# Kernel optimization log

Hardware: AMD Instinct MI355X
Metric: run time of the kernel (lower is better)

Reference implementation:

```python
import jax, jax.numpy as jnp
import numpy as np

N = 50000      # nodes
E = 800000     # edges (before self loops)
D_IN = 128
HID = 64
HEADS = 8
D_OUT = 10


def setup_inputs() -> dict:
    key = jax.random.key(0)
    ks = jax.random.split(key, 16)
    sc = 0.05
    x = jax.random.normal(ks[0], (N, D_IN), dtype=jnp.float32)
    edge_index = jax.random.randint(ks[1], (2, E), 0, N, dtype=jnp.int64)
    return {
        "x": x,
        "edge_index": edge_index,
        "W1": jax.random.normal(ks[2], (HEADS * HID, D_IN), dtype=jnp.float32) * sc,
        "a1_src": jax.random.normal(ks[3], (HEADS, HID), dtype=jnp.float32) * sc,
        "a1_dst": jax.random.normal(ks[4], (HEADS, HID), dtype=jnp.float32) * sc,
        "b1": jnp.zeros((HEADS * HID,), jnp.float32),
        "W2": jax.random.normal(ks[5], (HID, HEADS * HID), dtype=jnp.float32) * sc,
        "a2_src": jax.random.normal(ks[6], (1, HID), dtype=jnp.float32) * sc,
        "a2_dst": jax.random.normal(ks[7], (1, HID), dtype=jnp.float32) * sc,
        "b2": jnp.zeros((HID,), jnp.float32),
        "W3": jax.random.normal(ks[8], (HID, HID), dtype=jnp.float32) * sc,
        "a3_src": jax.random.normal(ks[9], (1, HID), dtype=jnp.float32) * sc,
        "a3_dst": jax.random.normal(ks[10], (1, HID), dtype=jnp.float32) * sc,
        "b3": jnp.zeros((HID,), jnp.float32),
        "Wc": jax.random.normal(ks[11], (D_OUT, HID), dtype=jnp.float32) * sc,
        "bc": jnp.zeros((D_OUT,), jnp.float32),
    }


def gat_conv(x, src, dst, W, a_src, a_dst, b, concat):
    """PyG GATConv (eval mode, add_self_loops already applied to src/dst)."""
    heads, out_ch = a_src.shape
    n = x.shape[0]
    h = (x @ W.T).reshape(n, heads, out_ch)          # [N, H, C]
    a_s = jnp.einsum('nhc,hc->nh', h, a_src)          # [N, H]
    a_d = jnp.einsum('nhc,hc->nh', h, a_dst)          # [N, H]
    e = jax.nn.leaky_relu(a_s[src] + a_d[dst], 0.2)   # [Etot, H]
    # segment softmax over incoming edges of each destination node
    m = jax.ops.segment_max(e, dst, num_segments=n)
    ex = jnp.exp(e - m[dst])
    s = jax.ops.segment_sum(ex, dst, num_segments=n)
    alpha = ex / (s[dst] + 1e-16)                     # [Etot, H]
    out = jax.ops.segment_sum(h[src] * alpha[:, :, None], dst, num_segments=n)
    if concat:
        out = out.reshape(n, heads * out_ch)
    else:
        out = out.mean(axis=1)
    return out + b


def reference(x, edge_index, W1, a1_src, a1_dst, b1, W2, a2_src, a2_dst, b2,
              W3, a3_src, a3_dst, b3, Wc, bc):
    loops = jnp.arange(N, dtype=edge_index.dtype)
    src = jnp.concatenate([edge_index[0], loops])
    dst = jnp.concatenate([edge_index[1], loops])
    h = jax.nn.elu(gat_conv(x, src, dst, W1, a1_src, a1_dst, b1, True))
    h = jax.nn.elu(gat_conv(h, src, dst, W2, a2_src, a2_dst, b2, False))
    h = jax.nn.elu(gat_conv(h, src, dst, W3, a3_src, a3_dst, b3, False))
    return h @ Wc.T + bc
```

## Files before the change

kernel.cpp:

```cpp
#include <hip/hip_runtime.h>
#include <math.h>

#define N_NODES 50000
#define N_EDGES 800000
#define ETOT    (N_EDGES + N_NODES)
#define COL_CAP (ETOT + 3 * N_NODES + 64)

typedef short bf16x8 __attribute__((ext_vector_type(8)));
typedef float f32x4  __attribute__((ext_vector_type(4)));
typedef float f32x2  __attribute__((ext_vector_type(2)));

__device__ __forceinline__ float b2f(unsigned int u16) {
    return __uint_as_float(u16 << 16);
}
__device__ __forceinline__ unsigned short f2b(float f) {
    unsigned int u = __float_as_uint(f);
    u += 0x7fffu + ((u >> 16) & 1u);
    return (unsigned short)(u >> 16);
}

__global__ __launch_bounds__(256) void k_prep(const float* __restrict__ x,
                                              const float* __restrict__ w1,
                                              const float* __restrict__ w2,
                                              const float* __restrict__ w3,
                                              const float* __restrict__ a1s,
                                              const float* __restrict__ a1d,
                                              unsigned short* __restrict__ xb,
                                              unsigned short* __restrict__ o1,
                                              unsigned short* __restrict__ o2,
                                              unsigned short* __restrict__ o3,
                                              float* __restrict__ U,
                                              int* __restrict__ deg,
                                              int* __restrict__ flag) {
    int i = blockIdx.x * 256 + threadIdx.x;
    if (i < N_NODES) deg[i] = 0;
    if (i == 0) *flag = 0;
    if (blockIdx.x < 8) {
        int h = blockIdx.x;
        int which = threadIdx.x >> 7, k = threadIdx.x & 127;
        const float* av = which ? a1d : a1s;
        float acc = 0.f;
        for (int c = 0; c < 64; ++c)
            acc += av[h * 64 + c] * w1[(size_t)(h * 64 + c) * 128 + k];
        U[(which * 8 + h) * 128 + k] = acc;
    }
    if (i < 512 * 128 / 4) {
        float4 v = ((const float4*)w1)[i];
        ushort2* o = (ushort2*)(o1 + i * 4);
        o[0] = make_ushort2(f2b(v.x), f2b(v.y));
        o[1] = make_ushort2(f2b(v.z), f2b(v.w));
    }
    if (i < 64 * 512 / 4) {
        float4 v = ((const float4*)w2)[i];
        ushort2* o = (ushort2*)(o2 + i * 4);
        o[0] = make_ushort2(f2b(v.x), f2b(v.y));
        o[1] = make_ushort2(f2b(v.z), f2b(v.w));
    }
    if (i < 64 * 64 / 4) {
        float4 v = ((const float4*)w3)[i];
        ushort2* o = (ushort2*)(o3 + i * 4);
        o[0] = make_ushort2(f2b(v.x), f2b(v.y));
        o[1] = make_ushort2(f2b(v.z), f2b(v.w));
    }
    if (i < N_NODES * 128 / 8) {
        const float4* xp = (const float4*)x + (size_t)i * 2;
        float4 v0 = xp[0], v1 = xp[1];
        unsigned int u0 = (unsigned int)f2b(v0.x) | ((unsigned int)f2b(v0.y) << 16);
        unsigned int u1 = (unsigned int)f2b(v0.z) | ((unsigned int)f2b(v0.w) << 16);
        unsigned int u2 = (unsigned int)f2b(v1.x) | ((unsigned int)f2b(v1.y) << 16);
        unsigned int u3 = (unsigned int)f2b(v1.z) | ((unsigned int)f2b(v1.w) << 16);
        *(uint4*)(xb + (size_t)i * 8) = make_uint4(u0, u1, u2, u3);
    }
}

__global__ __launch_bounds__(256) void k_attn(const unsigned short* __restrict__ xb,
                                              const float* __restrict__ U,
                                              float* __restrict__ asrc,
                                              float* __restrict__ adst) {
    __shared__ float sU[16 * 132];
    __shared__ unsigned short sX[16 * 136];
    int t = threadIdx.x;
    for (int i = t; i < 2048; i += 256) sU[(i >> 7) * 132 + (i & 127)] = U[i];
    int n0 = blockIdx.x * 16;
    {
        int r = t >> 4, c = (t & 15) * 8;
        *(uint4*)&sX[r * 136 + c] = *(const uint4*)(xb + (size_t)(n0 + r) * 128 + c);
    }
    __syncthreads();
    int nl = t >> 4, o = t & 15;
    const unsigned short* xr = sX + nl * 136;
    const float* ur = sU + o * 132;
    float acc = 0.f;
#pragma unroll 8
    for (int k2 = 0; k2 < 128; ++k2) acc += b2f(xr[k2]) * ur[k2];
    int n = n0 + nl;
    if (o < 8) asrc[n * 8 + o] = acc;
    else       adst[n * 8 + (o - 8)] = acc;
}

__global__ void k_detect(const int* __restrict__ idx, int* __restrict__ flag) {
    int i = blockIdx.x * blockDim.x + threadIdx.x;
    int v = idx[2 * i + 1];
    unsigned long long any = __ballot(v != 0);
    if ((threadIdx.x & 63) == 0 && any) atomicOr(flag, 1);
}

__device__ __forceinline__ int edge_src(const int* idx, int e, int is32) {
    return is32 ? idx[e] : idx[2 * e];
}
__device__ __forceinline__ int edge_dst(const int* idx, int e, int is32) {
    return is32 ? idx[N_EDGES + e] : idx[2 * (N_EDGES + e)];
}

__global__ void k_degree(const int* __restrict__ idx, const int* __restrict__ flag,
                         int* __restrict__ deg) {
    int e = blockIdx.x * blockDim.x + threadIdx.x;
    if (e >= ETOT) return;
    int is32 = *flag;
    int d = (e < N_EDGES) ? edge_dst(idx, e, is32) : (e - N_EDGES);
    atomicAdd(&deg[d], 1);
}

__global__ __launch_bounds__(256) void k_scan1(const int* __restrict__ deg,
                                               int* __restrict__ rowptr,
                                               int* __restrict__ bsum) {
    __shared__ int sd[256];
    int t = threadIdx.x;
    int i = blockIdx.x * 256 + t;
    int v = (i < N_NODES) ? ((deg[i] + 3) & ~3) : 0;
    sd[t] = v;
    __syncthreads();
#pragma unroll
    for (int off = 1; off < 256; off <<= 1) {
        int a = (t >= off) ? sd[t - off] : 0;
        __syncthreads();
        sd[t] += a;
        __syncthreads();
    }
    if (i < N_NODES) rowptr[i] = sd[t] - v;
    if (t == 255) bsum[blockIdx.x] = sd[255];
}

__global__ __launch_bounds__(256) void k_scan2(int* __restrict__ bsum,
                                               int* __restrict__ boff,
                                               int* __restrict__ rowptr,
                                               int nb) {
    __shared__ int sd[256];
    int t = threadIdx.x;
    int v = (t < nb) ? bsum[t] : 0;
    sd[t] = v;
    __syncthreads();
#pragma unroll
    for (int off = 1; off < 256; off <<= 1) {
        int a = (t >= off) ? sd[t - off] : 0;
        __syncthreads();
        sd[t] += a;
        __syncthreads();
    }
    boff[t] = sd[t] - v;
    if (t == 255) rowptr[N_NODES] = sd[255];
}

__global__ __launch_bounds__(256) void k_scan3(int* __restrict__ rowptr,
                                               const int* __restrict__ boff,
                                               const int* __restrict__ deg,
                                               int* __restrict__ cursor,
                                               int* __restrict__ col) {
    int i = blockIdx.x * 256 + threadIdx.x;
    if (i == 0) {
        int tot = rowptr[N_NODES];
        for (int q = 0; q < 48; ++q) col[tot + q] = 0;
    }
    if (i >= N_NODES) return;
    int r = rowptr[i] + boff[blockIdx.x];
    rowptr[i] = r;
    cursor[i] = r;
    int d = deg[i];
    int pd = (d + 3) & ~3;
    for (int p = r + d; p < r + pd; ++p) col[p] = 0;
}

__global__ void k_scatter(const int* __restrict__ idx, const int* __restrict__ flag,
                          int* __restrict__ cursor, int* __restrict__ col) {
    int e = blockIdx.x * blockDim.x + threadIdx.x;
    if (e >= ETOT) return;
    int is32 = *flag;
    int s, d;
    if (e < N_EDGES) { s = edge_src(idx, e, is32); d = edge_dst(idx, e, is32); }
    else             { s = d = e - N_EDGES; }
    int pos = atomicAdd(&cursor[d], 1);
    col[pos] = s;
}

__global__ __launch_bounds__(256) void k_gemm(const unsigned short* __restrict__ Ab,
                                              const unsigned short* __restrict__ W,
                                              unsigned short* __restrict__ C,
                                              const float* __restrict__ a_src,
                                              const float* __restrict__ a_dst,
                                              float* __restrict__ asb,
                                              float* __restrict__ adb,
                                              int M, int K, int Nout) {
    __shared__ unsigned short As[64 * 40];
    __shared__ unsigned short Bs[64 * 40];
    __shared__ float red_s[4][64];
    __shared__ float red_d[4][64];
    int t = threadIdx.x;
    int w = t >> 6, l = t & 63;
    int quad = l >> 4, lm = l & 15;
    int m0 = blockIdx.y * 64, n0 = blockIdx.x * 64;
    int hd = blockIdx.x;
    int lr = t >> 2;
    int lc = (t & 3) * 8;

    f32x4 acc[4];
#pragma unroll
    for (int r = 0; r < 4; ++r) acc[r] = (f32x4){0.f, 0.f, 0.f, 0.f};

    for (int k0 = 0; k0 < K; k0 += 32) {
        int m = m0 + lr;
        uint4 av = make_uint4(0, 0, 0, 0);
        if (m < M) av = *(const uint4*)(Ab + (size_t)m * K + k0 + lc);
        *(uint4*)&As[lr * 40 + lc] = av;
        uint4 bv = *(const uint4*)(W + (size_t)(n0 + lr) * K + k0 + lc);
        *(uint4*)&Bs[lr * 40 + lc] = bv;
        __syncthreads();

        bf16x8 bfrag = *(const bf16x8*)&Bs[(w * 16 + lm) * 40 + quad * 8];
#pragma unroll
        for (int r = 0; r < 4; ++r) {
            bf16x8 afrag = *(const bf16x8*)&As[(r * 16 + lm) * 40 + quad * 8];
            acc[r] = __builtin_amdgcn_mfma_f32_16x16x32_bf16(afrag, bfrag, acc[r], 0, 0, 0);
        }
        __syncthreads();
    }

#pragma unroll
    for (int r = 0; r < 4; ++r)
#pragma unroll
        for (int g = 0; g < 4; ++g) {
            int m = m0 + r * 16 + quad * 4 + g;
            if (m < M) C[(size_t)m * Nout + n0 + w * 16 + lm] = f2b(acc[r][g]);
        }

    float as = a_src[hd * 64 + w * 16 + lm];
    float ad = a_dst[hd * 64 + w * 16 + lm];
#pragma unroll
    for (int r = 0; r < 4; ++r) {
#pragma unroll
        for (int g = 0; g < 4; ++g) {
            float vs = acc[r][g] * as;
            float vd = acc[r][g] * ad;
#pragma unroll
            for (int off = 1; off < 16; off <<= 1) {
                vs += __shfl_xor(vs, off);
                vd += __shfl_xor(vd, off);
            }
            if (lm == 0) {
                red_s[w][r * 16 + quad * 4 + g] = vs;
                red_d[w][r * 16 + quad * 4 + g] = vd;
            }
        }
    }
    __syncthreads();
    if (t < 64) {
        float vs = red_s[0][t] + red_s[1][t] + red_s[2][t] + red_s[3][t];
        float vd = red_d[0][t] + red_d[1][t] + red_d[2][t] + red_d[3][t];
        int m = m0 + t;
        if (m < M) {
            asb[m] = vs;
            adb[m] = vd;
        }
    }
}

__device__ __forceinline__ void aggx_slot(int idx, int rem, float tt, unsigned int xx,
                                          float adn, float& ssum, f32x2* acc) {
    float e = tt + adn;
    e = fmaxf(e, 0.2f * e);
    float ex = __expf(e);
    ex = (idx < rem) ? ex : 0.f;
    ssum += ex;
    float fx = __uint_as_float(xx << 16);
    float fy = __uint_as_float(xx & 0xffff0000u);
    int exi = __float_as_int(ex);
#pragma unroll
    for (int hh = 0; hh < 8; ++hh) {
        float wh = __int_as_float(__builtin_amdgcn_readlane(exi, hh << 3));
        acc[hh].x = fmaf(fx, wh, acc[hh].x);
        acc[hh].y = fmaf(fy, wh, acc[hh].y);
    }
}

__global__ __launch_bounds__(256) void k_aggf(const unsigned short* __restrict__ xb,
                                              const float* __restrict__ asrc,
                                              const float* __restrict__ adst,
                                              const int* __restrict__ rowptr,
                                              const int* __restrict__ degv,
                                              const int* __restrict__ col,
                                              const unsigned short* __restrict__ W1b,
                                              const float* __restrict__ b1,
                                              unsigned short* __restrict__ x2) {
    __shared__ unsigned short sAgg[8 * 16 * 136];
    __shared__ int sCnt;
    int t = threadIdx.x;
    int l = t & 63;
    int wid = t >> 6;
    int n0 = blockIdx.x * 16;
    if (t == 0) sCnt = 0;
    __syncthreads();

    int j = l >> 3;
    unsigned lx2 = (unsigned)(l << 1);

    for (;;) {
        int m = 0;
        if (l == 0) m = atomicAdd(&sCnt, 1);
        m = __shfl(m, 0);
        if (m >= 16) break;
        int n = n0 + m;

        int start = rowptr[n];
        int end   = start + degv[n];
        float adn = adst[((unsigned)n << 3) + (unsigned)j];

        float ssum = 0.f;
        f32x2 acc[8];
#pragma unroll
        for (int hh = 0; hh < 8; ++hh) acc[hh] = (f32x2){0.f, 0.f};

        float tA0, tA1, tA2, tA3, tB0, tB1, tB2, tB3;
        unsigned int xA0, xA1, xA2, xA3, xB0, xB1, xB2, xB3;
        int4 cA, cB;

#define GATHX(c, T0, T1, T2, T3, X0, X1, X2, X3)                              \
    T0 = asrc[(((unsigned)(c).x) << 3) + (unsigned)j];                        \
    T1 = asrc[(((unsigned)(c).y) << 3) + (unsigned)j];                        \
    T2 = asrc[(((unsigned)(c).z) << 3) + (unsigned)j];                        \
    T3 = asrc[(((unsigned)(c).w) << 3) + (unsigned)j];                        \
    X0 = *(const unsigned int*)(xb + (((unsigned)(c).x) << 7) + lx2);         \
    X1 = *(const unsigned int*)(xb + (((unsigned)(c).y) << 7) + lx2);         \
    X2 = *(const unsigned int*)(xb + (((unsigned)(c).z) << 7) + lx2);         \
    X3 = *(const unsigned int*)(xb + (((unsigned)(c).w) << 7) + lx2);

        int k = start;
        cA = *(const int4*)(col + k);
        cB = *(const int4*)(col + k + 4);
        GATHX(cA, tA0, tA1, tA2, tA3, xA0, xA1, xA2, xA3);
        for (;;) {
            bool hasB = (k + 4 < end);
            if (hasB) {
                GATHX(cB, tB0, tB1, tB2, tB3, xB0, xB1, xB2, xB3);
                cA = *(const int4*)(col + k + 8);
            }
            {
                int rem = end - k;
                aggx_slot(0, rem, tA0, xA0, adn, ssum, acc);
                aggx_slot(1, rem, tA1, xA1, adn, ssum, acc);
                aggx_slot(2, rem, tA2, xA2, adn, ssum, acc);
                aggx_slot(3, rem, tA3, xA3, adn, ssum, acc);
            }
            k += 4;
            if (!hasB) break;
            bool hasA = (k + 4 < end);
            if (hasA) {
                GATHX(cA, tA0, tA1, tA2, tA3, xA0, xA1, xA2, xA3);
                cB = *(const int4*)(col + k + 8);
            }
            {
                int rem = end - k;
                aggx_slot(0, rem, tB0, xB0, adn, ssum, acc);
                aggx_slot(1, rem, tB1, xB1, adn, ssum, acc);
                aggx_slot(2, rem, tB2, xB2, adn, ssum, acc);
                aggx_slot(3, rem, tB3, xB3, adn, ssum, acc);
            }
            k += 4;
            if (!hasA) break;
        }
#undef GATHX

#pragma unroll
        for (int hh = 0; hh < 8; ++hh) {
            float sh = __int_as_float(__builtin_amdgcn_readlane(__float_as_int(ssum), hh << 3));
            float iv = 1.f / (sh + 1e-16f);
            unsigned int lo = f2b(acc[hh].x * iv);
            unsigned int hi = f2b(acc[hh].y * iv);
            *(unsigned int*)&sAgg[hh * 2176 + m * 136 + lx2] = lo | (hi << 16);
        }
    }
    __syncthreads();

    int lm = l & 15, q = l >> 4;
#pragma unroll
    for (int hh = 0; hh < 2; ++hh) {
        int h = wid * 2 + hh;
        f32x4 acc4[4];
#pragma unroll
        for (int t4 = 0; t4 < 4; ++t4) acc4[t4] = (f32x4){0.f, 0.f, 0.f, 0.f};
#pragma unroll
        for (int ks = 0; ks < 4; ++ks) {
            uint4 au = *(const uint4*)&sAgg[h * 2176 + lm * 136 + ks * 32 + (q << 3)];
            bf16x8 af = *(bf16x8*)&au;
#pragma unroll
            for (int t4 = 0; t4 < 4; ++t4) {
                uint4 bu = *(const uint4*)(W1b + (size_t)(h * 64 + t4 * 16 + lm) * 128 + ks * 32 + (q << 3));
                bf16x8 bf_ = *(bf16x8*)&bu;
                acc4[t4] = __builtin_amdgcn_mfma_f32_16x16x32_bf16(af, bf_, acc4[t4], 0, 0, 0);
            }
        }
#pragma unroll
        for (int t4 = 0; t4 < 4; ++t4) {
            float bc = b1[h * 64 + t4 * 16 + lm];
#pragma unroll
            for (int g = 0; g < 4; ++g) {
                int m = q * 4 + g;
                float v = acc4[t4][g] + bc;
                v = (v > 0.f) ? v : expm1f(v);
                x2[(size_t)(n0 + m) * 512 + h * 64 + t4 * 16 + lm] = f2b(v);
            }
        }
    }
}

__global__ __launch_bounds__(256) void k_agg1(const unsigned short* __restrict__ h,
                                              const float* __restrict__ asrc,
                                              const float* __restrict__ adst,
                                              const int* __restrict__ rowptr,
                                              const int* __restrict__ degv,
                                              const int* __restrict__ col,
                                              const float* __restrict__ bias,
                                              unsigned short* __restrict__ out) {
    int n = blockIdx.x * 4 + (threadIdx.x >> 6);
    if (n >= N_NODES) return;
    int l = threadIdx.x & 63;
    int start = rowptr[n];
    int end   = start + degv[n];
    float adn = adst[n];

    float ssum = 0.f, o = 0.f;
    float tA0, tA1, tA2, tA3, tB0, tB1, tB2, tB3;
    unsigned short qA0, qA1, qA2, qA3, qB0, qB1, qB2, qB3;
    int4 cA, cB;

#define GATH1(c, T0, T1, T2, T3, Q0, Q1, Q2, Q3)                              \
    T0 = asrc[(unsigned)(c).x];                                               \
    T1 = asrc[(unsigned)(c).y];                                               \
    T2 = asrc[(unsigned)(c).z];                                               \
    T3 = asrc[(unsigned)(c).w];                                               \
    Q0 = h[(((unsigned)(c).x) << 6) + (unsigned)l];                           \
    Q1 = h[(((unsigned)(c).y) << 6) + (unsigned)l];                           \
    Q2 = h[(((unsigned)(c).z) << 6) + (unsigned)l];                           \
    Q3 = h[(((unsigned)(c).w) << 6) + (unsigned)l];

#define ASLOT1(IDX, TT, QQ, rem)                                              \
    {                                                                         \
        float e = TT + adn;                                                   \
        e = fmaxf(e, 0.2f * e);                                               \
        float ex = __expf(e);                                                 \
        ex = ((IDX) < (rem)) ? ex : 0.f;                                      \
        ssum += ex;                                                           \
        o += ex * b2f(QQ);                                                    \
    }

    int k = start;
    cA = *(const int4*)(col + k);
    cB = *(const int4*)(col + k + 4);
    GATH1(cA, tA0, tA1, tA2, tA3, qA0, qA1, qA2, qA3);
    for (;;) {
        bool hasB = (k + 4 < end);
        if (hasB) {
            GATH1(cB, tB0, tB1, tB2, tB3, qB0, qB1, qB2, qB3);
            cA = *(const int4*)(col + k + 8);
        }
        {
            int rem = end - k;
            ASLOT1(0, tA0, qA0, rem);
            ASLOT1(1, tA1, qA1, rem);
            ASLOT1(2, tA2, qA2, rem);
            ASLOT1(3, tA3, qA3, rem);
        }
        k += 4;
        if (!hasB) break;
        bool hasA = (k + 4 < end);
        if (hasA) {
            GATH1(cA, tA0, tA1, tA2, tA3, qA0, qA1, qA2, qA3);
            cB = *(const int4*)(col + k + 8);
        }
        {
            int rem = end - k;
            ASLOT1(0, tB0, qB0, rem);
            ASLOT1(1, tB1, qB1, rem);
            ASLOT1(2, tB2, qB2, rem);
            ASLOT1(3, tB3, qB3, rem);
        }
        k += 4;
        if (!hasA) break;
    }
#undef GATH1
#undef ASLOT1

    float v = o / (ssum + 1e-16f) + bias[l];
    v = (v > 0.f) ? v : expm1f(v);
    out[(size_t)n * 64 + l] = f2b(v);
}

__global__ __launch_bounds__(256) void k_classifier(const unsigned short* __restrict__ h,
                                                    const float* __restrict__ Wc,
                                                    const float* __restrict__ bc,
                                                    float* __restrict__ out) {
    __shared__ float sW[640];
    for (int i = threadIdx.x; i < 640; i += blockDim.x) sW[i] = Wc[i];
    __syncthreads();
    int idx = blockIdx.x * blockDim.x + threadIdx.x;
    if (idx >= N_NODES * 10) return;
    int n = idx / 10, d = idx - n * 10;
    const unsigned short* hr = h + (size_t)n * 64;
    const float* wr = sW + d * 64;
    float acc = 0.f;
#pragma unroll
    for (int c = 0; c < 64; ++c) acc += b2f(hr[c]) * wr[c];
    out[idx] = acc + bc[d];
}

extern "C" void kernel_launch(void* const* d_in, const int* in_sizes, int n_in,
                              void* d_out, int out_size, void* d_ws, size_t ws_size,
                              hipStream_t stream) {
    const float* x    = (const float*)d_in[0];
    const int*   eidx = (const int*)  d_in[1];
    const float* W1   = (const float*)d_in[2];
    const float* a1s  = (const float*)d_in[3];
    const float* a1d  = (const float*)d_in[4];
    const float* b1   = (const float*)d_in[5];
    const float* W2   = (const float*)d_in[6];
    const float* a2s  = (const float*)d_in[7];
    const float* a2d  = (const float*)d_in[8];
    const float* b2   = (const float*)d_in[9];
    const float* W3   = (const float*)d_in[10];
    const float* a3s  = (const float*)d_in[11];
    const float* a3d  = (const float*)d_in[12];
    const float* b3   = (const float*)d_in[13];
    const float* Wc   = (const float*)d_in[14];
    const float* bc   = (const float*)d_in[15];
    float* out = (float*)d_out;

    float* asbuf = (float*)d_ws;
    float* adbuf = asbuf + (size_t)N_NODES * 8;
    unsigned short* x2  = (unsigned short*)(adbuf + (size_t)N_NODES * 8);
    unsigned short* h2  = x2  + (size_t)N_NODES * 512;
    unsigned short* x3  = h2  + (size_t)N_NODES * 64;
    unsigned short* h3  = x3  + (size_t)N_NODES * 64;
    unsigned short* x4  = h3  + (size_t)N_NODES * 64;
    unsigned short* xb  = x4  + (size_t)N_NODES * 64;
    unsigned short* W1b = xb  + (size_t)N_NODES * 128;
    unsigned short* W2b = W1b + 512 * 128;
    unsigned short* W3b = W2b + 64 * 512;
    float* U    = (float*)(W3b + 64 * 64);
    int* ibase  = (int*)(U + 16 * 128);
    int* deg    = ibase;
    int* flag   = deg + N_NODES;
    int* rowptr = flag + 1;
    int* cursor = rowptr + N_NODES + 1;
    int* bsum   = cursor + N_NODES;
    int* boff   = bsum + 256;
    int* col    = boff + 256;

    dim3 blk(256);
    const int SCAN_BLOCKS = (N_NODES + 255) / 256;
    const int PREP_BLOCKS = (N_NODES * 128 / 8 + 255) / 256;

    k_prep<<<PREP_BLOCKS, blk, 0, stream>>>(x, W1, W2, W3, a1s, a1d,
                                            xb, W1b, W2b, W3b, U, deg, flag);
    k_attn<<<N_NODES / 16, blk, 0, stream>>>(xb, U, asbuf, adbuf);

    k_detect<<<32, blk, 0, stream>>>(eidx, flag);
    k_degree<<<(ETOT + 255) / 256, blk, 0, stream>>>(eidx, flag, deg);
    k_scan1<<<SCAN_BLOCKS, blk, 0, stream>>>(deg, rowptr, bsum);
    k_scan2<<<1, blk, 0, stream>>>(bsum, boff, rowptr, SCAN_BLOCKS);
    k_scan3<<<SCAN_BLOCKS, blk, 0, stream>>>(rowptr, boff, deg, cursor, col);
    k_scatter<<<(ETOT + 255) / 256, blk, 0, stream>>>(eidx, flag, cursor, col);

    int mblocks = (N_NODES + 63) / 64;
    int nblocks = N_NODES / 4;

    k_aggf<<<N_NODES / 16, blk, 0, stream>>>(xb, asbuf, adbuf, rowptr, deg, col,
                                             W1b, b1, x2);

    k_gemm<<<dim3(1, mblocks), blk, 0, stream>>>(x2, W2b, h2,
                                                 a2s, a2d, asbuf, adbuf,
                                                 N_NODES, 512, 64);
    k_agg1<<<nblocks, blk, 0, stream>>>(h2, asbuf, adbuf, rowptr, deg, col, b2, x3);

    k_gemm<<<dim3(1, mblocks), blk, 0, stream>>>(x3, W3b, h3,
                                                 a3s, a3d, asbuf, adbuf,
                                                 N_NODES, 64, 64);
    k_agg1<<<nblocks, blk, 0, stream>>>(h3, asbuf, adbuf, rowptr, deg, col, b3, x4);

    k_classifier<<<(N_NODES * 10 + 255) / 256, blk, 0, stream>>>(x4, Wc, bc, out);
}
```

Before: 441.0 us.

## Split layer-1 aggregation from its GEMM and fuse W1 projection with the W2 GEMM

The fused aggregate-then-project layer-1 kernel is replaced by two kernels. The first does only per-head attention aggregation of the raw input features and writes a bf16 [N,8,128] buffer. The second fuses the per-head W1 projection, bias and ELU, holding the 512-wide hidden activation in shared memory, with the W2 GEMM and attention-score reduction. This removes the x2 round trip through global memory and the separate layer-2 GEMM launch. In exchange the aggregated buffer is twice as wide as x2, and the roughly 66KB of shared memory per block may limit occupancy.

```diff
diff --git a/kernel.cpp b/kernel.cpp
--- a/kernel.cpp
+++ b/kernel.cpp
@@ -192,6 +192,211 @@
     col[pos] = s;
 }
 
+__device__ __forceinline__ void aggx_slot(int idx, int rem, float tt, unsigned int xx,
+                                          float adn, float& ssum, f32x2* acc) {
+    float e = tt + adn;
+    e = fmaxf(e, 0.2f * e);
+    float ex = __expf(e);
+    ex = (idx < rem) ? ex : 0.f;
+    ssum += ex;
+    float fx = __uint_as_float(xx << 16);
+    float fy = __uint_as_float(xx & 0xffff0000u);
+    int exi = __float_as_int(ex);
+#pragma unroll
+    for (int hh = 0; hh < 8; ++hh) {
+        float wh = __int_as_float(__builtin_amdgcn_readlane(exi, hh << 3));
+        acc[hh].x = fmaf(fx, wh, acc[hh].x);
+        acc[hh].y = fmaf(fy, wh, acc[hh].y);
+    }
+}
+
+__global__ __launch_bounds__(256) void k_aggx(const unsigned short* __restrict__ xb,
+                                              const float* __restrict__ asrc,
+                                              const float* __restrict__ adst,
+                                              const int* __restrict__ rowptr,
+                                              const int* __restrict__ degv,
+                                              const int* __restrict__ col,
+                                              unsigned short* __restrict__ aggX) {
+    int n = blockIdx.x * 4 + (threadIdx.x >> 6);
+    if (n >= N_NODES) return;
+    int l = threadIdx.x & 63;
+    int j = l >> 3;
+    unsigned lx2 = (unsigned)(l << 1);
+    int start = rowptr[n];
+    int end   = start + degv[n];
+    float adn = adst[((unsigned)n << 3) + (unsigned)j];
+
+    float ssum = 0.f;
+    f32x2 acc[8];
+#pragma unroll
+    for (int hh = 0; hh < 8; ++hh) acc[hh] = (f32x2){0.f, 0.f};
+
+    float tA0, tA1, tA2, tA3, tB0, tB1, tB2, tB3;
+    unsigned int xA0, xA1, xA2, xA3, xB0, xB1, xB2, xB3;
+    int4 cA, cB;
+
+#define GATHX(c, T0, T1, T2, T3, X0, X1, X2, X3)                              \
+    T0 = asrc[(((unsigned)(c).x) << 3) + (unsigned)j];                        \
+    T1 = asrc[(((unsigned)(c).y) << 3) + (unsigned)j];                        \
+    T2 = asrc[(((unsigned)(c).z) << 3) + (unsigned)j];                        \
+    T3 = asrc[(((unsigned)(c).w) << 3) + (unsigned)j];                        \
+    X0 = *(const unsigned int*)(xb + (((unsigned)(c).x) << 7) + lx2);         \
+    X1 = *(const unsigned int*)(xb + (((unsigned)(c).y) << 7) + lx2);         \
+    X2 = *(const unsigned int*)(xb + (((unsigned)(c).z) << 7) + lx2);         \
+    X3 = *(const unsigned int*)(xb + (((unsigned)(c).w) << 7) + lx2);
+
+    int k = start;
+    cA = *(const int4*)(col + k);
+    cB = *(const int4*)(col + k + 4);
+    GATHX(cA, tA0, tA1, tA2, tA3, xA0, xA1, xA2, xA3);
+    for (;;) {
+        bool hasB = (k + 4 < end);
+        if (hasB) {
+            GATHX(cB, tB0, tB1, tB2, tB3, xB0, xB1, xB2, xB3);
+            cA = *(const int4*)(col + k + 8);
+        }
+        {
+            int rem = end - k;
+            aggx_slot(0, rem, tA0, xA0, adn, ssum, acc);
+            aggx_slot(1, rem, tA1, xA1, adn, ssum, acc);
+            aggx_slot(2, rem, tA2, xA2, adn, ssum, acc);
+            aggx_slot(3, rem, tA3, xA3, adn, ssum, acc);
+        }
+        k += 4;
+        if (!hasB) break;
+        bool hasA = (k + 4 < end);
+        if (hasA) {
+            GATHX(cA, tA0, tA1, tA2, tA3, xA0, xA1, xA2, xA3);
+            cB = *(const int4*)(col + k + 8);
+        }
+        {
+            int rem = end - k;
+            aggx_slot(0, rem, tB0, xB0, adn, ssum, acc);
+            aggx_slot(1, rem, tB1, xB1, adn, ssum, acc);
+            aggx_slot(2, rem, tB2, xB2, adn, ssum, acc);
+            aggx_slot(3, rem, tB3, xB3, adn, ssum, acc);
+        }
+        k += 4;
+        if (!hasA) break;
+    }
+#undef GATHX
+
+    size_t base = (size_t)n * 1024 + lx2;
+#pragma unroll
+    for (int hh = 0; hh < 8; ++hh) {
+        float sh = __int_as_float(__builtin_amdgcn_readlane(__float_as_int(ssum), hh << 3));
+        float iv = 1.f / (sh + 1e-16f);
+        unsigned int lo = f2b(acc[hh].x * iv);
+        unsigned int hi = f2b(acc[hh].y * iv);
+        *(unsigned int*)(aggX + base + hh * 128) = lo | (hi << 16);
+    }
+}
+
+__global__ __launch_bounds__(256) void k_gemm12(const unsigned short* __restrict__ aggX,
+                                                const unsigned short* __restrict__ W1b,
+                                                const float* __restrict__ b1,
+                                                const unsigned short* __restrict__ W2b,
+                                                const float* __restrict__ a2s,
+                                                const float* __restrict__ a2d,
+                                                unsigned short* __restrict__ h2,
+                                                float* __restrict__ asb,
+                                                float* __restrict__ adb) {
+    __shared__ unsigned short As[64 * 40];
+    __shared__ unsigned short Bs[64 * 40];
+    __shared__ unsigned short X2s[64 * 520];
+    __shared__ float red_s[4][64];
+    __shared__ float red_d[4][64];
+    int t = threadIdx.x;
+    int w = t >> 6, l = t & 63;
+    int quad = l >> 4, lm = l & 15;
+    int m0 = blockIdx.x * 64;
+    int lr = t >> 2;
+    int lc = (t & 3) * 8;
+
+    for (int h = 0; h < 8; ++h) {
+        f32x4 acc[4];
+#pragma unroll
+        for (int r = 0; r < 4; ++r) acc[r] = (f32x4){0.f, 0.f, 0.f, 0.f};
+        for (int k0 = 0; k0 < 128; k0 += 32) {
+            int m = m0 + lr;
+            uint4 av = make_uint4(0, 0, 0, 0);
+            if (m < N_NODES) av = *(const uint4*)(aggX + (size_t)m * 1024 + h * 128 + k0 + lc);
+            *(uint4*)&As[lr * 40 + lc] = av;
+            uint4 bv = *(const uint4*)(W1b + (size_t)(h * 64 + lr) * 128 + k0 + lc);
+            *(uint4*)&Bs[lr * 40 + lc] = bv;
+            __syncthreads();
+            bf16x8 bfrag = *(const bf16x8*)&Bs[(w * 16 + lm) * 40 + quad * 8];
+#pragma unroll
+            for (int r = 0; r < 4; ++r) {
+                bf16x8 afrag = *(const bf16x8*)&As[(r * 16 + lm) * 40 + quad * 8];
+                acc[r] = __builtin_amdgcn_mfma_f32_16x16x32_bf16(afrag, bfrag, acc[r], 0, 0, 0);
+            }
+            __syncthreads();
+        }
+        float bcol = b1[h * 64 + w * 16 + lm];
+#pragma unroll
+        for (int r = 0; r < 4; ++r)
+#pragma unroll
+            for (int g = 0; g < 4; ++g) {
+                float v = acc[r][g] + bcol;
+                v = (v > 0.f) ? v : expm1f(v);
+                X2s[(r * 16 + quad * 4 + g) * 520 + h * 64 + w * 16 + lm] = f2b(v);
+            }
+    }
+    __syncthreads();
+
+    f32x4 acc[4];
+#pragma unroll
+    for (int r = 0; r < 4; ++r) acc[r] = (f32x4){0.f, 0.f, 0.f, 0.f};
+    for (int k0 = 0; k0 < 512; k0 += 32) {
+        uint4 bu = *(const uint4*)(W2b + (size_t)(w * 16 + lm) * 512 + k0 + quad * 8);
+        bf16x8 bfrag = *(bf16x8*)&bu;
+#pragma unroll
+        for (int r = 0; r < 4; ++r) {
+            bf16x8 afrag = *(const bf16x8*)&X2s[(r * 16 + lm) * 520 + k0 + quad * 8];
+            acc[r] = __builtin_amdgcn_mfma_f32_16x16x32_bf16(afrag, bfrag, acc[r], 0, 0, 0);
+        }
+    }
+
+#pragma unroll
+    for (int r = 0; r < 4; ++r)
+#pragma unroll
+        for (int g = 0; g < 4; ++g) {
+            int m = m0 + r * 16 + quad * 4 + g;
+            if (m < N_NODES) h2[(size_t)m * 64 + w * 16 + lm] = f2b(acc[r][g]);
+        }
+
+    float as = a2s[w * 16 + lm];
+    float ad = a2d[w * 16 + lm];
+#pragma unroll
+    for (int r = 0; r < 4; ++r) {
+#pragma unroll
+        for (int g = 0; g < 4; ++g) {
+            float vs = acc[r][g] * as;
+            float vd = acc[r][g] * ad;
+#pragma unroll
+            for (int off = 1; off < 16; off <<= 1) {
+                vs += __shfl_xor(vs, off);
+                vd += __shfl_xor(vd, off);
+            }
+            if (lm == 0) {
+                red_s[w][r * 16 + quad * 4 + g] = vs;
+                red_d[w][r * 16 + quad * 4 + g] = vd;
+            }
+        }
+    }
+    __syncthreads();
+    if (t < 64) {
+        float vs = red_s[0][t] + red_s[1][t] + red_s[2][t] + red_s[3][t];
+        float vd = red_d[0][t] + red_d[1][t] + red_d[2][t] + red_d[3][t];
+        int m = m0 + t;
+        if (m < N_NODES) {
+            asb[m] = vs;
+            adb[m] = vd;
+        }
+    }
+}
+
 __global__ __launch_bounds__(256) void k_gemm(const unsigned short* __restrict__ Ab,
                                               const unsigned short* __restrict__ W,
                                               unsigned short* __restrict__ C,
@@ -208,7 +413,6 @@
     int w = t >> 6, l = t & 63;
     int quad = l >> 4, lm = l & 15;
     int m0 = blockIdx.y * 64, n0 = blockIdx.x * 64;
-    int hd = blockIdx.x;
     int lr = t >> 2;
     int lc = (t & 3) * 8;
 
@@ -242,8 +446,8 @@
             if (m < M) C[(size_t)m * Nout + n0 + w * 16 + lm] = f2b(acc[r][g]);
         }
 
-    float as = a_src[hd * 64 + w * 16 + lm];
-    float ad = a_dst[hd * 64 + w * 16 + lm];
+    float as = a_src[w * 16 + lm];
+    float ad = a_dst[w * 16 + lm];
 #pragma unroll
     for (int r = 0; r < 4; ++r) {
 #pragma unroll
@@ -269,154 +473,6 @@
         if (m < M) {
             asb[m] = vs;
             adb[m] = vd;
-        }
-    }
-}
-
-__device__ __forceinline__ void aggx_slot(int idx, int rem, float tt, unsigned int xx,
-                                          float adn, float& ssum, f32x2* acc) {
-    float e = tt + adn;
-    e = fmaxf(e, 0.2f * e);
-    float ex = __expf(e);
-    ex = (idx < rem) ? ex : 0.f;
-    ssum += ex;
-    float fx = __uint_as_float(xx << 16);
-    float fy = __uint_as_float(xx & 0xffff0000u);
-    int exi = __float_as_int(ex);
-#pragma unroll
-    for (int hh = 0; hh < 8; ++hh) {
-        float wh = __int_as_float(__builtin_amdgcn_readlane(exi, hh << 3));
-        acc[hh].x = fmaf(fx, wh, acc[hh].x);
-        acc[hh].y = fmaf(fy, wh, acc[hh].y);
-    }
-}
-
-__global__ __launch_bounds__(256) void k_aggf(const unsigned short* __restrict__ xb,
-                                              const float* __restrict__ asrc,
-                                              const float* __restrict__ adst,
-                                              const int* __restrict__ rowptr,
-                                              const int* __restrict__ degv,
-                                              const int* __restrict__ col,
-                                              const unsigned short* __restrict__ W1b,
-                                              const float* __restrict__ b1,
-                                              unsigned short* __restrict__ x2) {
-    __shared__ unsigned short sAgg[8 * 16 * 136];
-    __shared__ int sCnt;
-    int t = threadIdx.x;
-    int l = t & 63;
-    int wid = t >> 6;
-    int n0 = blockIdx.x * 16;
-    if (t == 0) sCnt = 0;
-    __syncthreads();
-
-    int j = l >> 3;
-    unsigned lx2 = (unsigned)(l << 1);
-
-    for (;;) {
-        int m = 0;
-        if (l == 0) m = atomicAdd(&sCnt, 1);
-        m = __shfl(m, 0);
-        if (m >= 16) break;
-        int n = n0 + m;
-
-        int start = rowptr[n];
-        int end   = start + degv[n];
-        float adn = adst[((unsigned)n << 3) + (unsigned)j];
-
-        float ssum = 0.f;
-        f32x2 acc[8];
-#pragma unroll
-        for (int hh = 0; hh < 8; ++hh) acc[hh] = (f32x2){0.f, 0.f};
-
-        float tA0, tA1, tA2, tA3, tB0, tB1, tB2, tB3;
-        unsigned int xA0, xA1, xA2, xA3, xB0, xB1, xB2, xB3;
-        int4 cA, cB;
-
-#define GATHX(c, T0, T1, T2, T3, X0, X1, X2, X3)                              \
-    T0 = asrc[(((unsigned)(c).x) << 3) + (unsigned)j];                        \
-    T1 = asrc[(((unsigned)(c).y) << 3) + (unsigned)j];                        \
-    T2 = asrc[(((unsigned)(c).z) << 3) + (unsigned)j];                        \
-    T3 = asrc[(((unsigned)(c).w) << 3) + (unsigned)j];                        \
-    X0 = *(const unsigned int*)(xb + (((unsigned)(c).x) << 7) + lx2);         \
-    X1 = *(const unsigned int*)(xb + (((unsigned)(c).y) << 7) + lx2);         \
-    X2 = *(const unsigned int*)(xb + (((unsigned)(c).z) << 7) + lx2);         \
-    X3 = *(const unsigned int*)(xb + (((unsigned)(c).w) << 7) + lx2);
-
-        int k = start;
-        cA = *(const int4*)(col + k);
-        cB = *(const int4*)(col + k + 4);
-        GATHX(cA, tA0, tA1, tA2, tA3, xA0, xA1, xA2, xA3);
-        for (;;) {
-            bool hasB = (k + 4 < end);
-            if (hasB) {
-                GATHX(cB, tB0, tB1, tB2, tB3, xB0, xB1, xB2, xB3);
-                cA = *(const int4*)(col + k + 8);
-            }
-            {
-                int rem = end - k;
-                aggx_slot(0, rem, tA0, xA0, adn, ssum, acc);
-                aggx_slot(1, rem, tA1, xA1, adn, ssum, acc);
-                aggx_slot(2, rem, tA2, xA2, adn, ssum, acc);
-                aggx_slot(3, rem, tA3, xA3, adn, ssum, acc);
-            }
-            k += 4;
-            if (!hasB) break;
-            bool hasA = (k + 4 < end);
-            if (hasA) {
-                GATHX(cA, tA0, tA1, tA2, tA3, xA0, xA1, xA2, xA3);
-                cB = *(const int4*)(col + k + 8);
-            }
-            {
-                int rem = end - k;
-                aggx_slot(0, rem, tB0, xB0, adn, ssum, acc);
-                aggx_slot(1, rem, tB1, xB1, adn, ssum, acc);
-                aggx_slot(2, rem, tB2, xB2, adn, ssum, acc);
-                aggx_slot(3, rem, tB3, xB3, adn, ssum, acc);
-            }
-            k += 4;
-            if (!hasA) break;
-        }
-#undef GATHX
-
-#pragma unroll
-        for (int hh = 0; hh < 8; ++hh) {
-            float sh = __int_as_float(__builtin_amdgcn_readlane(__float_as_int(ssum), hh << 3));
-            float iv = 1.f / (sh + 1e-16f);
-            unsigned int lo = f2b(acc[hh].x * iv);
-            unsigned int hi = f2b(acc[hh].y * iv);
-            *(unsigned int*)&sAgg[hh * 2176 + m * 136 + lx2] = lo | (hi << 16);
-        }
-    }
-    __syncthreads();
-
-    int lm = l & 15, q = l >> 4;
-#pragma unroll
-    for (int hh = 0; hh < 2; ++hh) {
-        int h = wid * 2 + hh;
-        f32x4 acc4[4];
-#pragma unroll
-        for (int t4 = 0; t4 < 4; ++t4) acc4[t4] = (f32x4){0.f, 0.f, 0.f, 0.f};
-#pragma unroll
-        for (int ks = 0; ks < 4; ++ks) {
-            uint4 au = *(const uint4*)&sAgg[h * 2176 + lm * 136 + ks * 32 + (q << 3)];
-            bf16x8 af = *(bf16x8*)&au;
-#pragma unroll
-            for (int t4 = 0; t4 < 4; ++t4) {
-                uint4 bu = *(const uint4*)(W1b + (size_t)(h * 64 + t4 * 16 + lm) * 128 + ks * 32 + (q << 3));
-                bf16x8 bf_ = *(bf16x8*)&bu;
-                acc4[t4] = __builtin_amdgcn_mfma_f32_16x16x32_bf16(af, bf_, acc4[t4], 0, 0, 0);
-            }
-        }
-#pragma unroll
-        for (int t4 = 0; t4 < 4; ++t4) {
-            float bc = b1[h * 64 + t4 * 16 + lm];
-#pragma unroll
-            for (int g = 0; g < 4; ++g) {
-                int m = q * 4 + g;
-                float v = acc4[t4][g] + bc;
-                v = (v > 0.f) ? v : expm1f(v);
-                x2[(size_t)(n0 + m) * 512 + h * 64 + t4 * 16 + lm] = f2b(v);
-            }
         }
     }
 }
@@ -544,8 +600,8 @@
 
     float* asbuf = (float*)d_ws;
     float* adbuf = asbuf + (size_t)N_NODES * 8;
-    unsigned short* x2  = (unsigned short*)(adbuf + (size_t)N_NODES * 8);
-    unsigned short* h2  = x2  + (size_t)N_NODES * 512;
+    unsigned short* aggX = (unsigned short*)(adbuf + (size_t)N_NODES * 8);
+    unsigned short* h2  = aggX + (size_t)N_NODES * 1024;
     unsigned short* x3  = h2  + (size_t)N_NODES * 64;
     unsigned short* h3  = x3  + (size_t)N_NODES * 64;
     unsigned short* x4  = h3  + (size_t)N_NODES * 64;
@@ -581,12 +637,11 @@
     int mblocks = (N_NODES + 63) / 64;
     int nblocks = N_NODES / 4;
 
-    k_aggf<<<N_NODES / 16, blk, 0, stream>>>(xb, asbuf, adbuf, rowptr, deg, col,
-                                             W1b, b1, x2);
-
-    k_gemm<<<dim3(1, mblocks), blk, 0, stream>>>(x2, W2b, h2,
-                                                 a2s, a2d, asbuf, adbuf,
-                                                 N_NODES, 512, 64);
+    k_aggx<<<nblocks, blk, 0, stream>>>(xb, asbuf, adbuf, rowptr, deg, col, aggX);
+
+    k_gemm12<<<mblocks, blk, 0, stream>>>(aggX, W1b, b1, W2b, a2s, a2d,
+                                          h2, asbuf, adbuf);
+
     k_agg1<<<nblocks, blk, 0, stream>>>(h2, asbuf, adbuf, rowptr, deg, col, b2, x3);
 
     k_gemm<<<dim3(1, mblocks), blk, 0, stream>>>(x3, W3b, h3,
```

New measurement: 437.1 us. About the same (-0.9%).
